# Kernel optimization log

Hardware: AMD Instinct MI355X
Metric: run time of the kernel (lower is better)

The kernel has to match this reference:

```python
import jax, jax.numpy as jnp
import numpy as np

NODE = 112
B = 4096
L1, L2, L3, L4 = 256, 256, 128, 64


def setup_inputs() -> dict:
    key = jax.random.key(0)
    ks = jax.random.split(key, 13)
    def lin(kw, kb, fan_in, fan_out):
        bound = 1.0 / np.sqrt(fan_in)
        W = jax.random.uniform(kw, (fan_out, fan_in), jnp.float32, -bound, bound)
        b = jax.random.uniform(kb, (fan_out,), jnp.float32, -bound, bound)
        return W, b
    x = jax.random.normal(ks[0], (B, NODE, NODE), jnp.float32)
    W1, b1 = lin(ks[1], ks[2], NODE, L1)
    W2, b2 = lin(ks[3], ks[4], L1, L2)
    W3, b3 = lin(ks[5], ks[6], L2, L3)
    W4, b4 = lin(ks[7], ks[8], L3, L4)
    W5, b5 = lin(ks[9], ks[10], L4, 1)
    Wf, bf = lin(ks[11], ks[12], NODE, 1)
    return {"x": x, "W1": W1, "b1": b1, "W2": W2, "b2": b2,
            "W3": W3, "b3": b3, "W4": W4, "b4": b4,
            "W5": W5, "b5": b5, "Wf": Wf, "bf": bf}


def reference(x, W1, b1, W2, b2, W3, b3, W4, b4, W5, b5, Wf, bf):
    # bmm(x, eye) == x, so first aggregation is the identity on x.
    h = x  # [B, node, node]
    # layer: aggregate via x, project, relu
    def layer(h, W, b):
        h = jnp.einsum('bnm,bmd->bnd', x, h)  # adjacency aggregation
        return jax.nn.relu(h @ W.T + b)
    h = jax.nn.relu(h @ W1.T + b1)            # first bmm is identity
    h = layer(h, W2, b2)
    h = layer(h, W3, b3)
    h = layer(h, W4, b4)
    h = layer(h, W5, b5)                      # [B, node, 1]
    h = h.reshape(h.shape[0], -1)             # [B, node]
    return h @ Wf.T + bf                      # [B, 1]
```

## Files before the change

kernel.cpp:

```cpp
#include <hip/hip_runtime.h>
#include <hip/hip_bf16.h>


#define NODE 112
#define NBATCH 4096
#define SXS 136
#define SAB 264
#define AB0_OFF 15232
#define AB1_OFF 44800
#define SMEM_BYTES ((AB1_OFF + 128*SAB)*2)

typedef float  f4v   __attribute__((ext_vector_type(4)));
typedef float  f16v  __attribute__((ext_vector_type(16)));
typedef __bf16 bf8v  __attribute__((ext_vector_type(8)));
typedef short  s8v   __attribute__((ext_vector_type(8)));
typedef unsigned u4v __attribute__((ext_vector_type(4)));
typedef unsigned short ushort_t;

__device__ __forceinline__ ushort_t f2bf(float f) {
  union { float f; unsigned u; } v; v.f = f;
  unsigned r = v.u + 0x7FFFu + ((v.u >> 16) & 1u);
  return (ushort_t)(r >> 16);
}
__device__ __forceinline__ float bf2f(ushort_t h) {
  union { unsigned u; float f; } v; v.u = ((unsigned)h) << 16; return v.f;
}
__device__ __forceinline__ unsigned pk2(float a, float b) {
  unsigned short ul = __builtin_bit_cast(unsigned short, (__bf16)a);
  unsigned short uh = __builtin_bit_cast(unsigned short, (__bf16)b);
  return (unsigned)ul | ((unsigned)uh << 16);
}
__device__ __forceinline__ bf8v ld_frag(const ushort_t* p) {
  s8v t = *(const s8v*)p;
  return __builtin_bit_cast(bf8v, t);
}
__device__ __forceinline__ unsigned xchg32(unsigned v, int lane) {
  return (unsigned)__builtin_amdgcn_ds_bpermute(((lane ^ 32) << 2), (int)v);
}
#define MFMA32(a,b,c) __builtin_amdgcn_mfma_f32_32x32x16_bf16((a),(b),(c),0,0,0)

template<int KS>
__device__ __forceinline__ void proj_exch(
    const ushort_t* aSrc, int sa,
    const ushort_t* __restrict__ Wg, int WK,
    const float* __restrict__ bias, int nt, int lane, unsigned* fr)
{
  const int l31 = lane & 31, h32 = lane >> 5;
  const bool hiH = (h32 != 0);

  f16v acc[4];
  #pragma unroll
  for (int m=0;m<4;m++)
    #pragma unroll
    for (int r=0;r<16;r++) acc[m][r] = 0.f;

  const ushort_t* aP = aSrc + l31*sa + h32*8;
  const ushort_t* bP = Wg + (nt*32 + l31)*WK + h32*8;
  #pragma unroll
  for (int ks=0; ks<KS; ks++) {
    bf8v B = ld_frag(bP + ks*16);
    #pragma unroll
    for (int m=0;m<4;m++)
      acc[m] = MFMA32(ld_frag(aP + m*32*sa + ks*16), B, acc[m]);
  }

  const float bv = bias[nt*32 + l31];
  #pragma unroll
  for (int m=0;m<4;m++) {
    unsigned P[4][2];
    const int NQ = (m==3) ? 2 : 4;
    #pragma unroll
    for (int q=0;q<4;q++) {
      if (q >= NQ) break;
      float v0 = fmaxf(acc[m][4*q+0]+bv, 0.f);
      float v1 = fmaxf(acc[m][4*q+1]+bv, 0.f);
      float v2 = fmaxf(acc[m][4*q+2]+bv, 0.f);
      float v3 = fmaxf(acc[m][4*q+3]+bv, 0.f);
      P[q][0] = pk2(v0, v1);
      P[q][1] = pk2(v2, v3);
    }
    {
      unsigned s0 = hiH ? P[0][0] : P[1][0];
      unsigned s1 = hiH ? P[0][1] : P[1][1];
      unsigned r0 = xchg32(s0, lane);
      unsigned r1 = xchg32(s1, lane);
      unsigned o0 = hiH ? P[1][0] : P[0][0];
      unsigned o1 = hiH ? P[1][1] : P[0][1];
      fr[8*m+0] = hiH ? r0 : o0;
      fr[8*m+1] = hiH ? r1 : o1;
      fr[8*m+2] = hiH ? o0 : r0;
      fr[8*m+3] = hiH ? o1 : r1;
    }
    if (m < 3) {
      unsigned s0 = hiH ? P[2][0] : P[3][0];
      unsigned s1 = hiH ? P[2][1] : P[3][1];
      unsigned r0 = xchg32(s0, lane);
      unsigned r1 = xchg32(s1, lane);
      unsigned o0 = hiH ? P[3][0] : P[2][0];
      unsigned o1 = hiH ? P[3][1] : P[2][1];
      fr[8*m+4] = hiH ? r0 : o0;
      fr[8*m+5] = hiH ? r1 : o1;
      fr[8*m+6] = hiH ? o0 : r0;
      fr[8*m+7] = hiH ? o1 : r1;
    }
  }
}

__device__ __forceinline__ void agg_store(
    const unsigned* fr, const ushort_t* Xs_, ushort_t* aDst, int mt, int lane)
{
  const int l31 = lane & 31, h32 = lane >> 5;

  f16v acc[4];
  #pragma unroll
  for (int n=0;n<4;n++)
    #pragma unroll
    for (int r=0;r<16;r++) acc[n][r] = 0.f;

  const ushort_t* bP = Xs_ + l31*SXS + h32*8;
  #pragma unroll
  for (int ks=0; ks<7; ks++) {
    u4v t = (u4v){fr[4*ks+0], fr[4*ks+1], fr[4*ks+2], fr[4*ks+3]};
    bf8v A = __builtin_bit_cast(bf8v, t);
    #pragma unroll
    for (int n=0;n<4;n++)
      acc[n] = MFMA32(A, ld_frag(bP + n*32*SXS + ks*16), acc[n]);
  }

  #pragma unroll
  for (int n=0;n<4;n++) {
    ushort_t* arow = aDst + (n*32 + l31)*SAB;
    bool on = (n < 3) || (l31 < 16);
    #pragma unroll
    for (int q=0;q<4;q++) {
      uint2 pv;
      pv.x = pk2(acc[n][4*q+0], acc[n][4*q+1]);
      pv.y = pk2(acc[n][4*q+2], acc[n][4*q+3]);
      if (on) *(uint2*)(arow + mt*32 + 8*q + 4*h32) = pv;
    }
  }
}

__global__ void prep_weights(const float* __restrict__ W1, const float* __restrict__ W2,
                             const float* __restrict__ W3, const float* __restrict__ W4,
                             ushort_t* __restrict__ o)
{
  int i = blockIdx.x*256 + threadIdx.x;
  if (i < 28672)       o[i] = f2bf(W1[i]);
  else if (i < 94208)  o[i] = f2bf(W2[i - 28672]);
  else if (i < 126976) o[i] = f2bf(W3[i - 94208]);
  else if (i < 135168) o[i] = f2bf(W4[i - 126976]);
}

__global__ void __launch_bounds__(512, 2) gcn_kernel(
    const float* __restrict__ x, const ushort_t* __restrict__ wsp,
    const float* __restrict__ b1, const float* __restrict__ b2,
    const float* __restrict__ b3, const float* __restrict__ b4,
    const float* __restrict__ W5, const float* __restrict__ b5,
    const float* __restrict__ Wf, const float* __restrict__ bfc,
    float* __restrict__ out)
{
  extern __shared__ ushort_t smem[];
  ushort_t* Xs  = smem;
  ushort_t* aB0 = smem + AB0_OFF;
  ushort_t* aB1 = smem + AB1_OFF;

  const int tid  = threadIdx.x;
  const int w    = tid >> 6;
  const int lane = tid & 63;

  {
    const float4* x4 = (const float4*)(x + (size_t)blockIdx.x * (NODE*NODE));
    for (int i = tid; i < (NODE*NODE/4); i += 512) {
      float4 v = x4[i];
      int r = i / 28, c4 = (i - r*28) * 4;
      uint2 pv; pv.x = pk2(v.x, v.y); pv.y = pk2(v.z, v.w);
      *(uint2*)(Xs + r*SXS + c4) = pv;
    }
  }
  __syncthreads();

  unsigned fr[28];

  proj_exch<7>(Xs, SXS, wsp, 112, b1, w, lane, fr);
  agg_store(fr, Xs, aB0, w, lane);
  __syncthreads();

  proj_exch<16>(aB0, SAB, wsp + 28672, 256, b2, w, lane, fr);
  agg_store(fr, Xs, aB1, w, lane);
  __syncthreads();

  if (w < 4) {
    proj_exch<16>(aB1, SAB, wsp + 94208, 256, b3, w, lane, fr);
    agg_store(fr, Xs, aB0, w, lane);
  }
  __syncthreads();

  if (w < 2) {
    proj_exch<8>(aB0, SAB, wsp + 126976, 128, b4, w, lane, fr);
    agg_store(fr, Xs, aB1, w, lane);
  }
  __syncthreads();

  float partial = 0.f;
  if (tid < NODE) {
    const ushort_t* row = aB1 + tid*SAB;
    float s = 0.f;
    #pragma unroll
    for (int k4 = 0; k4 < 16; k4++) {
      uint2 u = *(const uint2*)(row + k4*4);
      s += bf2f((ushort_t)(u.x & 0xFFFF)) * W5[k4*4+0];
      s += bf2f((ushort_t)(u.x >> 16))    * W5[k4*4+1];
      s += bf2f((ushort_t)(u.y & 0xFFFF)) * W5[k4*4+2];
      s += bf2f((ushort_t)(u.y >> 16))    * W5[k4*4+3];
    }
    s += b5[0];
    s = s > 0.f ? s : 0.f;
    partial = s * Wf[tid];
  }
  float* red = (float*)Xs;
  if (tid < 128) red[tid] = partial;
  __syncthreads();
  if (w == 0) {
    float v = red[lane] + red[lane + 64];
    #pragma unroll
    for (int off = 32; off > 0; off >>= 1)
      v += __shfl_xor(v, off, 64);
    if (lane == 0) out[blockIdx.x] = v + bfc[0];
  }
}

extern "C" void kernel_launch(void* const* d_in, const int* in_sizes, int n_in,
                              void* d_out, int out_size, void* d_ws, size_t ws_size,
                              hipStream_t stream) {
  const float* x   = (const float*)d_in[0];
  const float* W1  = (const float*)d_in[1];
  const float* b1  = (const float*)d_in[2];
  const float* W2  = (const float*)d_in[3];
  const float* b2  = (const float*)d_in[4];
  const float* W3  = (const float*)d_in[5];
  const float* b3  = (const float*)d_in[6];
  const float* W4  = (const float*)d_in[7];
  const float* b4  = (const float*)d_in[8];
  const float* W5  = (const float*)d_in[9];
  const float* b5  = (const float*)d_in[10];
  const float* Wf  = (const float*)d_in[11];
  const float* bfc = (const float*)d_in[12];
  ushort_t* wsp = (ushort_t*)d_ws;
  float* out = (float*)d_out;

  prep_weights<<<528, 256, 0, stream>>>(W1, W2, W3, W4, wsp);

  (void)hipFuncSetAttribute((const void*)gcn_kernel,
                            hipFuncAttributeMaxDynamicSharedMemorySize, SMEM_BYTES);
  gcn_kernel<<<NBATCH, 512, SMEM_BYTES, stream>>>(x, wsp, b1, b2, b3, b4,
                                                  W5, b5, Wf, bfc, out);
}
```

Baseline: 595.5 us.

## Hold adjacency fragments in registers and shrink LDS footprint

```diff
diff --git a/kernel.cpp b/kernel.cpp
--- a/kernel.cpp
+++ b/kernel.cpp
@@ -6,9 +6,8 @@
 #define NBATCH 4096
 #define SXS 136
 #define SAB 264
-#define AB0_OFF 15232
-#define AB1_OFF 44800
-#define SMEM_BYTES ((AB1_OFF + 128*SAB)*2)
+#define AB1_OFF 29568
+#define SMEM_BYTES (2*112*SAB*2)
 
 typedef float  f4v   __attribute__((ext_vector_type(4)));
 typedef float  f16v  __attribute__((ext_vector_type(16)));
@@ -39,32 +38,10 @@
 }
 #define MFMA32(a,b,c) __builtin_amdgcn_mfma_f32_32x32x16_bf16((a),(b),(c),0,0,0)
 
-template<int KS>
-__device__ __forceinline__ void proj_exch(
-    const ushort_t* aSrc, int sa,
-    const ushort_t* __restrict__ Wg, int WK,
-    const float* __restrict__ bias, int nt, int lane, unsigned* fr)
-{
-  const int l31 = lane & 31, h32 = lane >> 5;
-  const bool hiH = (h32 != 0);
-
-  f16v acc[4];
-  #pragma unroll
-  for (int m=0;m<4;m++)
-    #pragma unroll
-    for (int r=0;r<16;r++) acc[m][r] = 0.f;
-
-  const ushort_t* aP = aSrc + l31*sa + h32*8;
-  const ushort_t* bP = Wg + (nt*32 + l31)*WK + h32*8;
-  #pragma unroll
-  for (int ks=0; ks<KS; ks++) {
-    bf8v B = ld_frag(bP + ks*16);
-    #pragma unroll
-    for (int m=0;m<4;m++)
-      acc[m] = MFMA32(ld_frag(aP + m*32*sa + ks*16), B, acc[m]);
-  }
-
-  const float bv = bias[nt*32 + l31];
+__device__ __forceinline__ void exch_build(const f16v* acc, float bv, int lane,
+                                           unsigned* fr)
+{
+  const bool hiH = (lane >> 5) != 0;
   #pragma unroll
   for (int m=0;m<4;m++) {
     unsigned P[4][2];
@@ -106,25 +83,71 @@
   }
 }
 
+__device__ __forceinline__ void proj1_exch(
+    const bf8v* Xr, const ushort_t* __restrict__ Wg,
+    const float* __restrict__ bias, int nt, int lane, unsigned* fr)
+{
+  const int l31 = lane & 31, h32 = lane >> 5;
+  f16v acc[4];
+  #pragma unroll
+  for (int m=0;m<4;m++)
+    #pragma unroll
+    for (int r=0;r<16;r++) acc[m][r] = 0.f;
+
+  const ushort_t* bP = Wg + (nt*32 + l31)*112 + h32*8;
+  #pragma unroll
+  for (int ks=0; ks<7; ks++) {
+    bf8v B = ld_frag(bP + ks*16);
+    #pragma unroll
+    for (int m=0;m<4;m++)
+      acc[m] = MFMA32(Xr[m*7+ks], B, acc[m]);
+  }
+  exch_build(acc, bias[nt*32 + l31], lane, fr);
+}
+
+template<int KS>
+__device__ __forceinline__ void proj_exch(
+    const ushort_t* aSrc, const ushort_t* __restrict__ Wg, int WK,
+    const float* __restrict__ bias, int nt, int lane, unsigned* fr)
+{
+  const int l31 = lane & 31, h32 = lane >> 5;
+  f16v acc[4];
+  #pragma unroll
+  for (int m=0;m<4;m++)
+    #pragma unroll
+    for (int r=0;r<16;r++) acc[m][r] = 0.f;
+
+  const ushort_t* aP  = aSrc + l31*SAB + h32*8;
+  const ushort_t* aP3 = aSrc + (96 + (l31 & 15))*SAB + h32*8;
+  const ushort_t* bP  = Wg + (nt*32 + l31)*WK + h32*8;
+  #pragma unroll
+  for (int ks=0; ks<KS; ks++) {
+    bf8v B = ld_frag(bP + ks*16);
+    acc[0] = MFMA32(ld_frag(aP +            ks*16), B, acc[0]);
+    acc[1] = MFMA32(ld_frag(aP + 32*SAB +   ks*16), B, acc[1]);
+    acc[2] = MFMA32(ld_frag(aP + 64*SAB +   ks*16), B, acc[2]);
+    acc[3] = MFMA32(ld_frag(aP3 +           ks*16), B, acc[3]);
+  }
+  exch_build(acc, bias[nt*32 + l31], lane, fr);
+}
+
 __device__ __forceinline__ void agg_store(
-    const unsigned* fr, const ushort_t* Xs_, ushort_t* aDst, int mt, int lane)
+    const unsigned* fr, const bf8v* Xr, ushort_t* aDst, int mt, int lane)
 {
   const int l31 = lane & 31, h32 = lane >> 5;
-
   f16v acc[4];
   #pragma unroll
   for (int n=0;n<4;n++)
     #pragma unroll
     for (int r=0;r<16;r++) acc[n][r] = 0.f;
 
-  const ushort_t* bP = Xs_ + l31*SXS + h32*8;
   #pragma unroll
   for (int ks=0; ks<7; ks++) {
     u4v t = (u4v){fr[4*ks+0], fr[4*ks+1], fr[4*ks+2], fr[4*ks+3]};
     bf8v A = __builtin_bit_cast(bf8v, t);
     #pragma unroll
     for (int n=0;n<4;n++)
-      acc[n] = MFMA32(A, ld_frag(bP + n*32*SXS + ks*16), acc[n]);
+      acc[n] = MFMA32(A, Xr[n*7+ks], acc[n]);
   }
 
   #pragma unroll
@@ -161,44 +184,59 @@
     float* __restrict__ out)
 {
   extern __shared__ ushort_t smem[];
-  ushort_t* Xs  = smem;
-  ushort_t* aB0 = smem + AB0_OFF;
+  ushort_t* aB0 = smem;
   ushort_t* aB1 = smem + AB1_OFF;
 
   const int tid  = threadIdx.x;
   const int w    = tid >> 6;
   const int lane = tid & 63;
+  const int l31  = lane & 31, h32 = lane >> 5;
 
   {
+    ushort_t* Xstg = aB1;
     const float4* x4 = (const float4*)(x + (size_t)blockIdx.x * (NODE*NODE));
     for (int i = tid; i < (NODE*NODE/4); i += 512) {
       float4 v = x4[i];
       int r = i / 28, c4 = (i - r*28) * 4;
       uint2 pv; pv.x = pk2(v.x, v.y); pv.y = pk2(v.z, v.w);
-      *(uint2*)(Xs + r*SXS + c4) = pv;
+      *(uint2*)(Xstg + r*SXS + c4) = pv;
+    }
+  }
+  __syncthreads();
+
+  bf8v Xr[28];
+  {
+    const ushort_t* Xstg = aB1;
+    #pragma unroll
+    for (int t=0;t<4;t++) {
+      int row = (t < 3) ? (t*32 + l31) : (96 + (l31 & 15));
+      const ushort_t* rp = Xstg + row*SXS + h32*8;
+      #pragma unroll
+      for (int ks=0;ks<7;ks++)
+        Xr[t*7+ks] = ld_frag(rp + ks*16);
     }
   }
   __syncthreads();
 
   unsigned fr[28];
 
-  proj_exch<7>(Xs, SXS, wsp, 112, b1, w, lane, fr);
-  agg_store(fr, Xs, aB0, w, lane);
-  __syncthreads();
-
-  proj_exch<16>(aB0, SAB, wsp + 28672, 256, b2, w, lane, fr);
-  agg_store(fr, Xs, aB1, w, lane);
+  proj1_exch(Xr, wsp, b1, w, lane, fr);
+  agg_store(fr, Xr, aB0, w, lane);
+  __syncthreads();
+
+  proj_exch<16>(aB0, wsp + 28672, 256, b2, w, lane, fr);
+  agg_store(fr, Xr, aB1, w, lane);
   __syncthreads();
 
   if (w < 4) {
-    proj_exch<16>(aB1, SAB, wsp + 94208, 256, b3, w, lane, fr);
-    agg_store(fr, Xs, aB0, w, lane);
+    proj_exch<16>(aB1, wsp + 94208, 256, b3, w, lane, fr);
+    agg_store(fr, Xr, aB0, w, lane);
   }
   __syncthreads();
 
   if (w < 2) {
-    proj_exch<8>(aB0, SAB, wsp + 126976, 128, b4, w, lane, fr);
-    agg_store(fr, Xs, aB1, w, lane);
+    proj_exch<8>(aB0, wsp + 126976, 128, b4, w, lane, fr);
+    agg_store(fr, Xr, aB1, w, lane);
   }
   __syncthreads();
 
@@ -218,7 +256,8 @@
     s = s > 0.f ? s : 0.f;
     partial = s * Wf[tid];
   }
-  float* red = (float*)Xs;
+  float* red = (float*)aB0;
+  __syncthreads();
   if (tid < 128) red[tid] = partial;
   __syncthreads();
   if (w == 0) {
```

Result: faster. 568.5 us (-4.5%).
